# Optimization experiments

Measured on AMD Instinct MI355X. Metric: run time of the kernel, lower is better.

Reference implementation:

```python
import jax, jax.numpy as jnp
import numpy as np

WIDTH = 16
N_LAYERS = 2
N_HIGHWAY = 2
B, S, D = 16, 2048, 512


def _causal_band(x, w):
    # out[:, t] = sum_{d=0..WIDTH} w[WIDTH-d] * x[:, t-d]  (x[<0]=0)
    out = w[WIDTH] * x
    for d in range(1, WIDTH + 1):
        out = out + w[WIDTH - d] * jnp.pad(x, ((0, 0), (d, 0), (0, 0)))[:, :S]
    return out


def _anticausal_band(x, w):
    # out[:, t] = sum_{d=0..WIDTH} w[d] * x[:, t+d]  (x[>=S]=0)
    out = w[0] * x
    for d in range(1, WIDTH + 1):
        out = out + w[d] * jnp.pad(x, ((0, 0), (0, d), (0, 0)))[:, d:]
    return out


def _highway(x, Ws, bs):
    # Ws: [N_HIGHWAY, D, 2D], bs: [N_HIGHWAY, 2D] (allennlp Highway, relu activation)
    for i in range(N_HIGHWAY):
        proj = jnp.einsum('bsd,de->bse', x, Ws[i]) + bs[i]
        nonlinear, gate = jnp.split(proj, 2, axis=-1)
        g = jax.nn.sigmoid(gate)
        x = g * x + (1.0 - g) * jax.nn.relu(nonlinear)
    return x


def setup_inputs() -> dict:
    key = jax.random.key(0)
    ks = jax.random.split(key, 8)
    scale = 1.0 / np.sqrt(D)
    return {
        'inputs': jax.random.normal(ks[0], (B, S, D), jnp.float32),
        'masks': jnp.ones((B, S), jnp.int32),
        'fw_band': jax.random.normal(ks[1], (N_LAYERS, WIDTH + 1), jnp.float32),
        'bw_band': jax.random.normal(ks[2], (N_LAYERS, WIDTH + 1), jnp.float32),
        'fw_W': jax.random.normal(ks[3], (N_LAYERS, N_HIGHWAY, D, 2 * D), jnp.float32) * scale,
        'fw_b': jax.random.normal(ks[4], (N_LAYERS, N_HIGHWAY, 2 * D), jnp.float32) * 0.1,
        'bw_W': jax.random.normal(ks[5], (N_LAYERS, N_HIGHWAY, D, 2 * D), jnp.float32) * scale,
        'bw_b': jax.random.normal(ks[6], (N_LAYERS, N_HIGHWAY, 2 * D), jnp.float32) * 0.1,
    }


def reference(inputs, masks, fw_band, bw_band, fw_W, fw_b, bw_W, bw_b):
    fwd = inputs
    bwd = inputs
    outs = []
    for l in range(N_LAYERS):
        fwd = _causal_band(fwd, fw_band[l])
        bwd = _anticausal_band(bwd, bw_band[l])
        fwd = _highway(fwd, fw_W[l], fw_b[l])
        bwd = _highway(bwd, bw_W[l], bw_b[l])
        outs.append(jnp.concatenate([fwd, bwd], axis=-1))
    return jnp.stack(outs, axis=0)  # [N_LAYERS, B, S, 2D]
```

## Files before the change

### kernel.cpp

```cpp
#include <hip/hip_runtime.h>
#include <hip/hip_bf16.h>

#define B_ 16
#define S_ 2048
#define D_ 512
#define M_ (B_ * S_)

typedef __attribute__((ext_vector_type(8))) _Float16 f16x8;
typedef __attribute__((ext_vector_type(4))) float f32x4;

#define GLOAD_LDS16(gp, lp)                                                   \
    __builtin_amdgcn_global_load_lds(                                         \
        (const __attribute__((address_space(1))) unsigned int*)(gp),          \
        (__attribute__((address_space(3))) unsigned int*)(lp), 16, 0, 0)

__global__ __launch_bounds__(256) void prep_w_kernel(
    const float* __restrict__ fwW, const float* __restrict__ bwW,
    _Float16* __restrict__ Wt)
{
    __shared__ float tile[32][33];
    int bid = blockIdx.x;
    int mat = bid >> 9;
    int t   = bid & 511;
    int kt  = t >> 5;
    int nt  = t & 31;
    int l   = mat >> 2;
    int dir = (mat >> 1) & 1;
    int h   = mat & 1;
    const float* src = (dir ? bwW : fwW) + (long long)(l * 2 + h) * (512LL * 1024);

    int tx = threadIdx.x & 31;
    int ty = threadIdx.x >> 5;
#pragma unroll
    for (int j = 0; j < 4; ++j) {
        int k = kt * 32 + ty + j * 8;
        tile[ty + j * 8][tx] = src[(long long)k * 1024 + nt * 32 + tx];
    }
    __syncthreads();
    _Float16* dst = Wt + (long long)mat * (1024LL * 512);
#pragma unroll
    for (int j = 0; j < 4; ++j) {
        int n = nt * 32 + ty + j * 8;
        dst[(long long)n * 512 + kt * 32 + tx] = (_Float16)tile[tx][ty + j * 8];
    }
}

__global__ __launch_bounds__(256) void band_conv_kernel(
    const float* __restrict__ src, long long bstride, int rstride,
    const float* __restrict__ w17, int causal,
    _Float16* __restrict__ Th)
{
    int id = blockIdx.x * 256 + threadIdx.x;
    int c  = id & (D_ - 1);
    int tt = (id >> 9) & (S_ / 4 - 1);
    int b  = id >> 18;
    int t0 = tt * 4;

    float w[17];
#pragma unroll
    for (int e = 0; e < 17; ++e) w[e] = w17[e];

    float buf[20];
    int tbase = t0 - (causal ? 16 : 0);
    const float* sp = src + (long long)b * bstride + c;
#pragma unroll
    for (int i = 0; i < 20; ++i) {
        int t = tbase + i;
        buf[i] = (t >= 0 && t < S_) ? sp[(long long)t * rstride] : 0.f;
    }
#pragma unroll
    for (int j = 0; j < 4; ++j) {
        float a = 0.f;
#pragma unroll
        for (int e = 0; e <= 16; ++e) a = fmaf(w[e], buf[j + e], a);
        Th[((long long)(b * S_ + t0 + j)) * D_ + c] = (_Float16)a;
    }
}

__global__ __launch_bounds__(512, 2) void hw_step_kernel(
    const _Float16* __restrict__ Xh,
    const _Float16* __restrict__ Wt,
    const float* __restrict__ bias,
    float* __restrict__ outF, int outF_stride,
    _Float16* __restrict__ outH)
{
    __shared__ _Float16 lds[65536];
    char* ldsb = (char*)lds;

    int tid = threadIdx.x;

    int f = blockIdx.x;
    int L = (f & 7) * 64 + (f >> 3);
    int colb = L & 3;
    int rowb = L >> 2;
    long long m0 = (long long)rowb * 256;
    int n0 = colb * 128;

    int lane = tid & 63;
    int wave = tid >> 6;
    int wave_m = wave >> 1;
    int wave_n = wave & 1;
    int wrow = wave_m * 64;
    int wn   = wave_n * 64;
    int ln = lane & 15;
    int q  = lane >> 4;

    int rloc  = tid >> 3;
    int cperm = 8 * ((tid & 7) ^ (rloc & 7));
    const _Float16* gA  = Xh + (m0 + rloc) * 512 + cperm;
    const _Float16* gBn = Wt + (long long)(n0 + rloc) * 512 + cperm;
    const _Float16* gBg = Wt + (long long)(512 + n0 + rloc) * 512 + cperm;

    auto stageA = [&](int b, int kt, int h2) {
#pragma unroll
        for (int j = 0; j < 2; ++j)
            GLOAD_LDS16(gA + (long long)(h2 * 128 + j * 64) * 512 + kt * 64,
                        ldsb + b * 32768 + h2 * 16384 + (j * 512 + tid) * 16);
    };
    auto stageB = [&](int b, int kt, int h2) {
        const _Float16* g = h2 ? gBg : gBn;
#pragma unroll
        for (int j = 0; j < 2; ++j)
            GLOAD_LDS16(g + (long long)(j * 64) * 512 + kt * 64,
                        ldsb + 65536 + b * 32768 + h2 * 16384 + (j * 512 + tid) * 16);
    };

    f32x4 acc[2][4][4];
#pragma unroll
    for (int h = 0; h < 2; ++h)
#pragma unroll
        for (int jn = 0; jn < 4; ++jn)
#pragma unroll
            for (int i = 0; i < 4; ++i) acc[h][jn][i] = (f32x4){0.f, 0.f, 0.f, 0.f};

    stageB(0, 0, 0);
    stageA(0, 0, 0);
    stageA(0, 0, 1);
    stageB(0, 0, 1);
    stageB(1, 1, 0);
    asm volatile("s_waitcnt vmcnt(2)" ::: "memory");
    __builtin_amdgcn_s_barrier();

    f16x8 af[4];
    for (int kt = 0; kt < 8; ++kt) {
        int b = kt & 1;
        const char* Ab = ldsb + b * 32768;
        const char* Bb = ldsb + 65536 + b * 32768;
#pragma unroll
        for (int p = 0; p < 4; ++p) {
            const int h = p & 1, ks = p >> 1;
            const int cb = ks * 64 + q * 16;
            if ((p & 1) == 0) {
#pragma unroll
                for (int i = 0; i < 4; ++i) {
                    int row = wrow + i * 16 + ln;
                    af[i] = *(const f16x8*)(Ab + row * 128 + (cb ^ ((row & 7) << 4)));
                }
            }
            f16x8 bf[4];
#pragma unroll
            for (int jn = 0; jn < 4; ++jn) {
                int row = h * 128 + wn + jn * 16 + ln;
                bf[jn] = *(const f16x8*)(Bb + row * 128 + (cb ^ ((row & 7) << 4)));
            }
            if (p == 0) { if (kt + 1 < 8) stageA(b ^ 1, kt + 1, 0); }
            if (p == 1) { if (kt + 1 < 8) stageA(b ^ 1, kt + 1, 1); }
            if (p == 2) { if (kt + 1 < 8) stageB(b ^ 1, kt + 1, 1); }
            if (p == 3) {
                if (kt + 2 < 8) stageB(b, kt + 2, 0);
                if (kt < 6)       asm volatile("s_waitcnt vmcnt(2)" ::: "memory");
                else if (kt == 6) asm volatile("s_waitcnt vmcnt(0)" ::: "memory");
            }
            __builtin_amdgcn_s_barrier();
            asm volatile("s_waitcnt lgkmcnt(0)" ::: "memory");
            __builtin_amdgcn_sched_barrier(0);
            __builtin_amdgcn_s_setprio(1);
#pragma unroll
            for (int jn = 0; jn < 4; ++jn)
#pragma unroll
                for (int i = 0; i < 4; ++i)
                    acc[h][jn][i] = __builtin_amdgcn_mfma_f32_16x16x32_f16(
                        af[i], bf[jn], acc[h][jn][i], 0, 0, 0);
            __builtin_amdgcn_s_setprio(0);
            __builtin_amdgcn_s_barrier();
        }
    }

#pragma unroll
    for (int j = 0; j < 8; ++j) {
        int idx = j * 512 + tid;
        int row = idx >> 4;
        int col = (idx & 15) * 8;
        GLOAD_LDS16(Xh + (m0 + row) * 512 + n0 + col, ldsb + idx * 16);
    }
    asm volatile("s_waitcnt vmcnt(0)" ::: "memory");
    __builtin_amdgcn_s_barrier();

#pragma unroll
    for (int jn = 0; jn < 4; ++jn) {
        int oc = wn + jn * 16 + ln;
        int c  = n0 + oc;
        float bnl = bias[c];
        float bg  = bias[512 + c];
#pragma unroll
        for (int i = 0; i < 4; ++i) {
#pragma unroll
            for (int r = 0; r < 4; ++r) {
                int xr = wrow + i * 16 + q * 4 + r;
                long long m = m0 + xr;
                float nl = acc[0][jn][i][r] + bnl;
                float gt = acc[1][jn][i][r] + bg;
                float g  = 1.f / (1.f + __expf(-gt));
                float xv = (float)lds[xr * 128 + oc];
                float o  = g * xv + (1.f - g) * fmaxf(nl, 0.f);
                if (outF) outF[m * (long long)outF_stride + c] = o;
                if (outH) outH[m * 512 + c] = (_Float16)o;
            }
        }
    }
}

extern "C" void kernel_launch(void* const* d_in, const int* in_sizes, int n_in,
                              void* d_out, int out_size, void* d_ws, size_t ws_size,
                              hipStream_t stream)
{
    const float* inputs  = (const float*)d_in[0];
    const float* fw_band = (const float*)d_in[2];
    const float* bw_band = (const float*)d_in[3];
    const float* fw_W    = (const float*)d_in[4];
    const float* fw_b    = (const float*)d_in[5];
    const float* bw_W    = (const float*)d_in[6];
    const float* bw_b    = (const float*)d_in[7];
    float* out = (float*)d_out;

    char* ws = (char*)d_ws;
    const size_t SZ_TH = (size_t)M_ * D_ * 2;
    _Float16* Th = (_Float16*)(ws);
    _Float16* Hh = (_Float16*)(ws + SZ_TH);
    _Float16* Wt = (_Float16*)(ws + 2 * SZ_TH);

    prep_w_kernel<<<4096, 256, 0, stream>>>(fw_W, bw_W, Wt);

    for (int l = 0; l < 2; ++l) {
        for (int dir = 0; dir < 2; ++dir) {
            const float* src; long long bstride; int rstride;
            if (l == 0) { src = inputs; bstride = (long long)S_ * D_; rstride = D_; }
            else {
                src = out + (long long)(l - 1) * M_ * 1024 + dir * 512;
                bstride = (long long)S_ * 1024; rstride = 1024;
            }
            const float* band = (dir ? bw_band : fw_band) + l * 17;
            band_conv_kernel<<<(B_ * (S_ / 4) * D_) / 256, 256, 0, stream>>>(
                src, bstride, rstride, band, dir == 0 ? 1 : 0, Th);

            const _Float16* W0 = Wt + (size_t)((l * 2 + dir) * 2 + 0) * (1024 * 512);
            const _Float16* W1 = Wt + (size_t)((l * 2 + dir) * 2 + 1) * (1024 * 512);
            const float* bias = (dir ? bw_b : fw_b) + (size_t)(l * 2) * 1024;

            hw_step_kernel<<<512, 512, 0, stream>>>(Th, W0, bias, nullptr, 0, Hh);
            float* oF = out + (long long)l * M_ * 1024 + dir * 512;
            hw_step_kernel<<<512, 512, 0, stream>>>(Hh, W1, bias + 1024, oF, 1024, nullptr);
        }
    }
}
```

Measured before the change: 821.3 us.

## Process two row tiles per highway block with continuous pipelined K loop

Each highway-step block now handles two consecutive 256-row panels (grid 512→256), running a single 16-step pipelined loop so the next panel's loads prefetch while the first panel's epilogue runs. The epilogue reads the residual X directly from global memory instead of staging it through LDS. Intent is to amortize prologue/pipeline fill and hide epilogue latency, at the cost of fewer blocks (256 on 256 CUs) and uncoalesced-ish global residual reads.

```diff
diff --git a/kernel.cpp b/kernel.cpp
--- a/kernel.cpp
+++ b/kernel.cpp
@@ -90,10 +90,10 @@
     int tid = threadIdx.x;
 
     int f = blockIdx.x;
-    int L = (f & 7) * 64 + (f >> 3);
+    int L = (f & 7) * 32 + (f >> 3);
     int colb = L & 3;
-    int rowb = L >> 2;
-    long long m0 = (long long)rowb * 256;
+    int rp   = L >> 2;
+    long long m0 = (long long)rp * 512;
     int n0 = colb * 128;
 
     int lane = tid & 63;
@@ -111,17 +111,19 @@
     const _Float16* gBn = Wt + (long long)(n0 + rloc) * 512 + cperm;
     const _Float16* gBg = Wt + (long long)(512 + n0 + rloc) * 512 + cperm;
 
-    auto stageA = [&](int b, int kt, int h2) {
+    auto stageA = [&](int b, int T1, int h2) {
+        long long roff =
+            (long long)((T1 >> 3) * 256 + h2 * 128) * 512 + (T1 & 7) * 64;
 #pragma unroll
         for (int j = 0; j < 2; ++j)
-            GLOAD_LDS16(gA + (long long)(h2 * 128 + j * 64) * 512 + kt * 64,
+            GLOAD_LDS16(gA + roff + (long long)(j * 64) * 512,
                         ldsb + b * 32768 + h2 * 16384 + (j * 512 + tid) * 16);
     };
-    auto stageB = [&](int b, int kt, int h2) {
+    auto stageB = [&](int b, int T1, int h2) {
         const _Float16* g = h2 ? gBg : gBn;
 #pragma unroll
         for (int j = 0; j < 2; ++j)
-            GLOAD_LDS16(g + (long long)(j * 64) * 512 + kt * 64,
+            GLOAD_LDS16(g + (long long)(j * 64) * 512 + (T1 & 7) * 64,
                         ldsb + 65536 + b * 32768 + h2 * 16384 + (j * 512 + tid) * 16);
     };
 
@@ -132,6 +134,30 @@
         for (int jn = 0; jn < 4; ++jn)
 #pragma unroll
             for (int i = 0; i < 4; ++i) acc[h][jn][i] = (f32x4){0.f, 0.f, 0.f, 0.f};
+
+    auto epilogue = [&](int pnl) {
+        long long mb = m0 + pnl * 256;
+#pragma unroll
+        for (int jn = 0; jn < 4; ++jn) {
+            int c = n0 + wn + jn * 16 + ln;
+            float bnl = bias[c];
+            float bg  = bias[512 + c];
+#pragma unroll
+            for (int i = 0; i < 4; ++i) {
+#pragma unroll
+                for (int r = 0; r < 4; ++r) {
+                    long long m = mb + wrow + i * 16 + q * 4 + r;
+                    float nl = acc[0][jn][i][r] + bnl;
+                    float gt = acc[1][jn][i][r] + bg;
+                    float g  = 1.f / (1.f + __expf(-gt));
+                    float xv = (float)Xh[m * 512 + c];
+                    float o  = g * xv + (1.f - g) * fmaxf(nl, 0.f);
+                    if (outF) outF[m * (long long)outF_stride + c] = o;
+                    if (outH) outH[m * 512 + c] = (_Float16)o;
+                }
+            }
+        }
+    };
 
     stageB(0, 0, 0);
     stageA(0, 0, 0);
@@ -142,8 +168,8 @@
     __builtin_amdgcn_s_barrier();
 
     f16x8 af[4];
-    for (int kt = 0; kt < 8; ++kt) {
-        int b = kt & 1;
+    for (int T = 0; T < 16; ++T) {
+        int b = T & 1;
         const char* Ab = ldsb + b * 32768;
         const char* Bb = ldsb + 65536 + b * 32768;
 #pragma unroll
@@ -163,14 +189,15 @@
                 int row = h * 128 + wn + jn * 16 + ln;
                 bf[jn] = *(const f16x8*)(Bb + row * 128 + (cb ^ ((row & 7) << 4)));
             }
-            if (p == 0) { if (kt + 1 < 8) stageA(b ^ 1, kt + 1, 0); }
-            if (p == 1) { if (kt + 1 < 8) stageA(b ^ 1, kt + 1, 1); }
-            if (p == 2) { if (kt + 1 < 8) stageB(b ^ 1, kt + 1, 1); }
+            if (p == 0) { if (T + 1 < 16) stageA(b ^ 1, T + 1, 0); }
+            if (p == 1) { if (T + 1 < 16) stageA(b ^ 1, T + 1, 1); }
+            if (p == 2) { if (T + 1 < 16) stageB(b ^ 1, T + 1, 1); }
             if (p == 3) {
-                if (kt + 2 < 8) stageB(b, kt + 2, 0);
-                if (kt < 6)       asm volatile("s_waitcnt vmcnt(2)" ::: "memory");
-                else if (kt == 6) asm volatile("s_waitcnt vmcnt(0)" ::: "memory");
-            }
+                if (T + 2 < 16) stageB(b, T + 2, 0);
+                if (T < 14)       asm volatile("s_waitcnt vmcnt(2)" ::: "memory");
+                else if (T == 14) asm volatile("s_waitcnt vmcnt(0)" ::: "memory");
+            }
+            __builtin_amdgcn_sched_barrier(0);
             __builtin_amdgcn_s_barrier();
             asm volatile("s_waitcnt lgkmcnt(0)" ::: "memory");
             __builtin_amdgcn_sched_barrier(0);
@@ -182,42 +209,21 @@
                     acc[h][jn][i] = __builtin_amdgcn_mfma_f32_16x16x32_f16(
                         af[i], bf[jn], acc[h][jn][i], 0, 0, 0);
             __builtin_amdgcn_s_setprio(0);
+            __builtin_amdgcn_sched_barrier(0);
             __builtin_amdgcn_s_barrier();
         }
-    }
-
-#pragma unroll
-    for (int j = 0; j < 8; ++j) {
-        int idx = j * 512 + tid;
-        int row = idx >> 4;
-        int col = (idx & 15) * 8;
-        GLOAD_LDS16(Xh + (m0 + row) * 512 + n0 + col, ldsb + idx * 16);
-    }
-    asm volatile("s_waitcnt vmcnt(0)" ::: "memory");
-    __builtin_amdgcn_s_barrier();
-
-#pragma unroll
-    for (int jn = 0; jn < 4; ++jn) {
-        int oc = wn + jn * 16 + ln;
-        int c  = n0 + oc;
-        float bnl = bias[c];
-        float bg  = bias[512 + c];
-#pragma unroll
-        for (int i = 0; i < 4; ++i) {
-#pragma unroll
-            for (int r = 0; r < 4; ++r) {
-                int xr = wrow + i * 16 + q * 4 + r;
-                long long m = m0 + xr;
-                float nl = acc[0][jn][i][r] + bnl;
-                float gt = acc[1][jn][i][r] + bg;
-                float g  = 1.f / (1.f + __expf(-gt));
-                float xv = (float)lds[xr * 128 + oc];
-                float o  = g * xv + (1.f - g) * fmaxf(nl, 0.f);
-                if (outF) outF[m * (long long)outF_stride + c] = o;
-                if (outH) outH[m * 512 + c] = (_Float16)o;
-            }
-        }
-    }
+        if (T == 7) {
+            epilogue(0);
+#pragma unroll
+            for (int h = 0; h < 2; ++h)
+#pragma unroll
+                for (int jn = 0; jn < 4; ++jn)
+#pragma unroll
+                    for (int i = 0; i < 4; ++i)
+                        acc[h][jn][i] = (f32x4){0.f, 0.f, 0.f, 0.f};
+        }
+    }
+    epilogue(1);
 }
 
 extern "C" void kernel_launch(void* const* d_in, const int* in_sizes, int n_in,
@@ -257,9 +263,9 @@
             const _Float16* W1 = Wt + (size_t)((l * 2 + dir) * 2 + 1) * (1024 * 512);
             const float* bias = (dir ? bw_b : fw_b) + (size_t)(l * 2) * 1024;
 
-            hw_step_kernel<<<512, 512, 0, stream>>>(Th, W0, bias, nullptr, 0, Hh);
+            hw_step_kernel<<<256, 512, 0, stream>>>(Th, W0, bias, nullptr, 0, Hh);
             float* oF = out + (long long)l * M_ * 1024 + dir * 512;
-            hw_step_kernel<<<512, 512, 0, stream>>>(Hh, W1, bias + 1024, oF, 1024, nullptr);
-        }
-    }
-}
+            hw_step_kernel<<<256, 512, 0, stream>>>(Hh, W1, bias + 1024, oF, 1024, nullptr);
+        }
+    }
+}
```

After: 1.108 ms. 1.35x slower.
